# Optimization experiments

Measured on AMD Instinct MI355X. Metric: run time of the kernel, lower is better.

## Reference

```python
import jax, jax.numpy as jnp
import numpy as np

N = 50000
E = 400000
D = 128   # embed_dim == per-head out_channels
H = 2     # graph_heads
NEG_SLOPE = 0.2


def setup_inputs() -> dict:
    key = jax.random.key(0)
    ks = jax.random.split(key, 10)
    s = 1.0 / np.sqrt(D)
    x = jax.random.normal(ks[0], (N, D), dtype=jnp.float32)
    edge_index = jax.random.randint(ks[1], (2, E), 0, N, dtype=jnp.int64)
    # GATv2Conv params: lin_l (source), lin_r (target), attention vector, conv bias
    Wl = jax.random.uniform(ks[2], (H * D, D), jnp.float32, -s, s)
    bl = jax.random.uniform(ks[3], (H * D,), jnp.float32, -s, s)
    Wr = jax.random.uniform(ks[4], (H * D, D), jnp.float32, -s, s)
    br = jax.random.uniform(ks[5], (H * D,), jnp.float32, -s, s)
    att = jax.random.uniform(ks[6], (H, D), jnp.float32, -s, s)
    bias_conv = jnp.zeros((H * D,), jnp.float32)
    # trailing Linear(H*D -> D)
    so = 1.0 / np.sqrt(H * D)
    Wo = jax.random.uniform(ks[7], (D, H * D), jnp.float32, -so, so)
    bo = jax.random.uniform(ks[8], (D,), jnp.float32, -so, so)
    return {"x": x, "edge_index": edge_index, "Wl": Wl, "bl": bl, "Wr": Wr,
            "br": br, "att": att, "bias_conv": bias_conv, "Wo": Wo, "bo": bo}


def reference(x, edge_index, Wl, bl, Wr, br, att, bias_conv, Wo, bo):
    n = x.shape[0]
    # GATv2Conv default add_self_loops=True
    loops = jnp.arange(n, dtype=edge_index.dtype)
    src = jnp.concatenate([edge_index[0], loops])  # x_j (source / message)
    dst = jnp.concatenate([edge_index[1], loops])  # x_i (target / aggregation)

    xl = (x @ Wl.T + bl).reshape(n, H, D)  # source projection
    xr = (x @ Wr.T + br).reshape(n, H, D)  # target projection

    e = xl[src] + xr[dst]                               # [E+N, H, D]
    score = jnp.einsum('ehd,hd->eh', jax.nn.leaky_relu(e, NEG_SLOPE), att)

    # segment softmax over destination neighborhoods
    m = jax.ops.segment_max(score, dst, num_segments=n)  # [N, H]
    a = jnp.exp(score - m[dst])
    denom = jax.ops.segment_sum(a, dst, num_segments=n)
    alpha = a / (denom[dst] + 1e-16)                     # [E+N, H]

    out = jax.ops.segment_sum(xl[src] * alpha[..., None], dst, num_segments=n)
    out = out.reshape(n, H * D) + bias_conv              # concat heads + conv bias
    return out @ Wo.T + bo                               # [N, D]
```

## Files before the change

kernel.cpp:

```cpp
#include <hip/hip_runtime.h>
#include <math.h>

#define DIMV 128
#define HDV  256
#define NEGS 0.2f
#define CAPV 64

typedef __attribute__((ext_vector_type(8))) short short8;
typedef __attribute__((ext_vector_type(8))) unsigned short ushort8v;
typedef __attribute__((ext_vector_type(4))) float f32x4;

__device__ __forceinline__ int edge_at(const int* p, int is64, long long idx) {
    return is64 ? p[2 * idx] : p[(size_t)idx];
}

__device__ __forceinline__ unsigned short f2bf(float f) {
    union { float f; unsigned u; } v; v.f = f;
    unsigned r = (v.u + 0x7FFF + ((v.u >> 16) & 1)) >> 16;
    return (unsigned short)r;
}
__device__ __forceinline__ float bf2f(unsigned short b) {
    union { unsigned u; float f; } v; v.u = ((unsigned)b) << 16;
    return v.f;
}

__global__ __launch_bounds__(256) void build_prep_kernel(
    const int* __restrict__ eidx, int E, int nn,
    int* __restrict__ deg, int* __restrict__ elist,
    const float* __restrict__ Wl, const float* __restrict__ Wr,
    const float* __restrict__ Wo,
    unsigned short* __restrict__ WB, unsigned short* __restrict__ WoB)
{
    const int b = blockIdx.x, t = threadIdx.x;
    if (b < 128) {
        int tid = b * 256 + t;
        int f = tid * 2;
        int e    = f & 7;
        int rowc = (f >> 3) & 127;
        int lg   = (f >> 10) & 3;
        int kk   = (f >> 12) & 3;
        int mh   = f >> 14;
        int mat = mh >> 1, half = mh & 1;
        const float* W = mat ? Wr : Wl;
        float2 v = *(const float2*)(W + (size_t)(half * 128 + rowc) * DIMV + kk * 32 + lg * 8 + e);
        ushort2 o; o.x = f2bf(v.x); o.y = f2bf(v.y);
        *(ushort2*)(WB + f) = o;
    } else if (b < 192) {
        int tid = (b - 128) * 256 + t;
        int f = tid * 2;
        int e    = f & 7;
        int rowc = (f >> 3) & 127;
        int lg   = (f >> 10) & 3;
        int kk   = f >> 12;
        float2 v = *(const float2*)(Wo + (size_t)rowc * HDV + kk * 32 + lg * 8 + e);
        ushort2 o; o.x = f2bf(v.x); o.y = f2bf(v.y);
        *(ushort2*)(WoB + f) = o;
    } else {
        const int idx = (b - 192) * 256 + t;
        const int Et = E + nn;
        if (idx >= Et) return;
        const int is64 = ((eidx[1] | eidx[3] | eidx[5] | eidx[7]) == 0) ? 1 : 0;
        int s, d;
        if (idx < E) {
            s = edge_at(eidx, is64, idx);
            d = edge_at(eidx, is64, (long long)E + idx);
        } else {
            s = idx - E; d = s;
        }
        int pos = atomicAdd(deg + d, 1);
        if (pos < CAPV) elist[(size_t)d * CAPV + pos] = s;
    }
}

__global__ __launch_bounds__(512) void proj_mfma_kernel(
    const float* __restrict__ x,
    const unsigned short* __restrict__ WB,
    const float* __restrict__ bl, const float* __restrict__ br,
    unsigned short* __restrict__ xl, unsigned short* __restrict__ xr, int nn)
{
    __shared__ __align__(16) unsigned short buf[32768];
    const int t = threadIdx.x;
    const int m0b = blockIdx.x * 64;
    const int lane = t & 63, w8 = t >> 6;
    const int w = w8 & 3, half = w8 >> 2;
    const int lm = lane & 15, lg = lane >> 4;

    const int rowi = min(m0b + w * 16 + lm, nn - 1);
    const float* arow_p = x + (size_t)rowi * DIMV;
    short8 af[4];
#pragma unroll
    for (int kk = 0; kk < 4; ++kk) {
        float4 v0 = *(const float4*)(arow_p + kk * 32 + lg * 8);
        float4 v1 = *(const float4*)(arow_p + kk * 32 + lg * 8 + 4);
        short8 a;
        a[0] = (short)f2bf(v0.x); a[1] = (short)f2bf(v0.y);
        a[2] = (short)f2bf(v0.z); a[3] = (short)f2bf(v0.w);
        a[4] = (short)f2bf(v1.x); a[5] = (short)f2bf(v1.y);
        a[6] = (short)f2bf(v1.z); a[7] = (short)f2bf(v1.w);
        af[kk] = a;
    }

    f32x4 acc0[8], acc1[8];
#pragma unroll
    for (int nt = 0; nt < 8; ++nt) {
        acc0[nt] = (f32x4){0.f, 0.f, 0.f, 0.f};
        acc1[nt] = (f32x4){0.f, 0.f, 0.f, 0.f};
    }

    const unsigned short* myhalf = buf + half * 16384;

    {
        const ushort8v* src = (const ushort8v*)WB;
        ushort8v* dst = (ushort8v*)buf;
        for (int i = t; i < 4096; i += 512) dst[i] = src[i];
    }
    __syncthreads();
#pragma unroll
    for (int kk = 0; kk < 4; ++kk) {
        const unsigned short* wbL = myhalf + (kk * 4 + lg) * 1024;
#pragma unroll
        for (int nt = 0; nt < 8; ++nt) {
            short8 b0 = *(const short8*)(wbL + (nt * 16 + lm) * 8);
            acc0[nt] = __builtin_amdgcn_mfma_f32_16x16x32_bf16(af[kk], b0, acc0[nt], 0, 0, 0);
        }
    }
    __syncthreads();
    {
        const ushort8v* src = (const ushort8v*)(WB + 32768);
        ushort8v* dst = (ushort8v*)buf;
        for (int i = t; i < 4096; i += 512) dst[i] = src[i];
    }
    __syncthreads();
#pragma unroll
    for (int kk = 0; kk < 4; ++kk) {
        const unsigned short* wbL = myhalf + (kk * 4 + lg) * 1024;
#pragma unroll
        for (int nt = 0; nt < 8; ++nt) {
            short8 b1 = *(const short8*)(wbL + (nt * 16 + lm) * 8);
            acc1[nt] = __builtin_amdgcn_mfma_f32_16x16x32_bf16(af[kk], b1, acc1[nt], 0, 0, 0);
        }
    }
    __syncthreads();

    const int colbase = half * 128;
#pragma unroll
    for (int nt = 0; nt < 8; ++nt) {
        const int c = colbase + nt * 16 + lm;
        const float bv = bl[c];
#pragma unroll
        for (int rg = 0; rg < 4; ++rg)
            buf[(w * 16 + lg * 4 + rg) * 256 + c] = f2bf(acc0[nt][rg] + bv);
    }
    __syncthreads();
    for (int i = t; i < 64 * 32; i += 512) {
        int rr = i >> 5, q = i & 31;
        if (m0b + rr < nn)
            *(ushort8v*)(xl + (size_t)(m0b + rr) * HDV + q * 8) =
                *(const ushort8v*)(buf + rr * 256 + q * 8);
    }
    __syncthreads();
#pragma unroll
    for (int nt = 0; nt < 8; ++nt) {
        const int c = colbase + nt * 16 + lm;
        const float bv = br[c];
#pragma unroll
        for (int rg = 0; rg < 4; ++rg)
            buf[(w * 16 + lg * 4 + rg) * 256 + c] = f2bf(acc1[nt][rg] + bv);
    }
    __syncthreads();
    for (int i = t; i < 64 * 32; i += 512) {
        int rr = i >> 5, q = i & 31;
        if (m0b + rr < nn)
            *(ushort8v*)(xr + (size_t)(m0b + rr) * HDV + q * 8) =
                *(const ushort8v*)(buf + rr * 256 + q * 8);
    }
}

__global__ __launch_bounds__(256) void fused_kernel(
    const unsigned short* __restrict__ xl, const unsigned short* __restrict__ xr,
    const float* __restrict__ att,
    const int* __restrict__ deg, const int* __restrict__ elist,
    const float* __restrict__ bias_conv,
    const unsigned short* __restrict__ WoB, const float* __restrict__ bo,
    float* __restrict__ out, int nn)
{
    __shared__ __align__(16) unsigned short ags[16 * 256];
    const int t = threadIdx.x, lane = t & 63, wid = t >> 6;
    const int h = lane & 31, par = lane >> 5;
    const int n0 = blockIdx.x * 16;
    char* agsb = (char*)ags;
    float att8[8], bc8[8];
#pragma unroll
    for (int k = 0; k < 8; ++k) {
        att8[k] = att[h * 8 + k];
        bc8[k]  = bias_conv[h * 8 + k];
    }

    for (int j = 0; j < 4; ++j) {
        const int n = n0 + wid * 4 + j;
        const int r = wid * 4 + j;
        int dg = 0;
        const int* __restrict__ row = elist;
        float xr8[8];
#pragma unroll
        for (int k = 0; k < 8; ++k) xr8[k] = 0.f;
        if (n < nn) {
            dg = min(deg[n], CAPV);
            row = elist + (size_t)n * CAPV;
            ushort8v v = *(const ushort8v*)(xr + (size_t)n * HDV + h * 8);
#pragma unroll
            for (int k = 0; k < 8; ++k) xr8[k] = bf2f(v[k]);
        }
        const int myidx = row[lane];
        const int np = (dg + 1) >> 1, np1 = np - 1, dgm1 = dg - 1;
        float m0 = -1e30f, den = 0.f;
        float a8[8];
#pragma unroll
        for (int k = 0; k < 8; ++k) a8[k] = 0.f;

        if (np > 0) {
            int i0 = __shfl(myidx, min(par, dgm1), 64);
            int i1 = __shfl(myidx, min(2 * min(1, np1) + par, dgm1), 64);
            int i2 = __shfl(myidx, min(2 * min(2, np1) + par, dgm1), 64);
            int i3 = __shfl(myidx, min(2 * min(3, np1) + par, dgm1), 64);
            ushort8v v0 = *(const ushort8v*)(xl + (size_t)i0 * HDV + h * 8);
            ushort8v v1 = *(const ushort8v*)(xl + (size_t)i1 * HDV + h * 8);
            ushort8v v2 = *(const ushort8v*)(xl + (size_t)i2 * HDV + h * 8);
            ushort8v v3 = *(const ushort8v*)(xl + (size_t)i3 * HDV + h * 8);
            for (int ip = 0; ip < np; ++ip) {
                ushort8v cur = v0; v0 = v1; v1 = v2; v2 = v3;
                {
                    int pn = min(2 * min(ip + 4, np1) + par, dgm1);
                    int in_ = __shfl(myidx, pn, 64);
                    v3 = *(const ushort8v*)(xl + (size_t)in_ * HDV + h * 8);
                }
                float xv8[8];
#pragma unroll
                for (int k = 0; k < 8; ++k) xv8[k] = bf2f(cur[k]);
                float p = 0.f;
#pragma unroll
                for (int k = 0; k < 8; ++k) {
                    float e = xv8[k] + xr8[k];
                    e = fmaxf(e, NEGS * e);
                    p = fmaf(e, att8[k], p);
                }
                p += __shfl_xor(p, 1);
                p += __shfl_xor(p, 2);
                p += __shfl_xor(p, 4);
                p += __shfl_xor(p, 8);
                const bool valid = (2 * ip + par) < dg;
                if (!valid) p = -1e30f;
                if (p > m0) {
                    float sc = __expf(m0 - p);
                    den *= sc;
#pragma unroll
                    for (int k = 0; k < 8; ++k) a8[k] *= sc;
                    m0 = p;
                }
                float wgt = valid ? __expf(p - m0) : 0.f;
                den += wgt;
#pragma unroll
                for (int k = 0; k < 8; ++k) a8[k] = fmaf(wgt, xv8[k], a8[k]);
            }
        }
        float m1 = __shfl_xor(m0, 32);
        float d1 = __shfl_xor(den, 32);
        float mm = fmaxf(m0, m1);
        float s0 = __expf(m0 - mm);
        den = den * s0 + d1 * __expf(m1 - mm);
        float rden = 1.f / (den + 1e-16f);
        ushort8v o;
#pragma unroll
        for (int k = 0; k < 8; ++k) {
            float as = a8[k] * s0;
            as += __shfl_xor(as, 32);
            o[k] = f2bf(fmaf(as, rden, bc8[k]));
        }
        if (par == 0)
            *(ushort8v*)(agsb + ((r * 512 + h * 16) ^ ((r & 7) << 4))) = o;
    }
    __syncthreads();

    const int lm = lane & 15, lg = lane >> 4;
    f32x4 acc2[2];
    acc2[0] = (f32x4){0.f, 0.f, 0.f, 0.f};
    acc2[1] = (f32x4){0.f, 0.f, 0.f, 0.f};
    const int aswz = (lm & 7) << 4;
#pragma unroll
    for (int kk = 0; kk < 8; ++kk) {
        short8 afrag = *(const short8*)(agsb + ((lm * 512 + kk * 64 + lg * 16) ^ aswz));
        const unsigned short* wb = WoB + (size_t)((kk * 4 + lg) * 128) * 8;
#pragma unroll
        for (int u = 0; u < 2; ++u) {
            const int brow = (wid * 2 + u) * 16 + lm;
            short8 bfrag = *(const short8*)(wb + brow * 8);
            acc2[u] = __builtin_amdgcn_mfma_f32_16x16x32_bf16(afrag, bfrag, acc2[u], 0, 0, 0);
        }
    }
#pragma unroll
    for (int u = 0; u < 2; ++u) {
        const int c = (wid * 2 + u) * 16 + lm;
        const float bv = bo[c];
#pragma unroll
        for (int rg = 0; rg < 4; ++rg) {
            const int node = n0 + lg * 4 + rg;
            if (node < nn) out[(size_t)node * DIMV + c] = acc2[u][rg] + bv;
        }
    }
}

extern "C" void kernel_launch(void* const* d_in, const int* in_sizes, int n_in,
                              void* d_out, int out_size, void* d_ws, size_t ws_size,
                              hipStream_t stream) {
    const float* x         = (const float*)d_in[0];
    const int*   eidx      = (const int*)d_in[1];
    const float* Wl        = (const float*)d_in[2];
    const float* bl        = (const float*)d_in[3];
    const float* Wr        = (const float*)d_in[4];
    const float* br        = (const float*)d_in[5];
    const float* att       = (const float*)d_in[6];
    const float* bias_conv = (const float*)d_in[7];
    const float* Wo        = (const float*)d_in[8];
    const float* bo        = (const float*)d_in[9];
    float* out = (float*)d_out;

    const int nn = in_sizes[0] / DIMV;
    const int E  = in_sizes[1] / 2;
    const int Et = E + nn;

    char* ws = (char*)d_ws;
    size_t off = 0;
    auto alloc = [&](size_t bytes) -> void* {
        void* p = ws + off;
        off += (bytes + 255) & ~(size_t)255;
        return p;
    };
    unsigned short* xl  = (unsigned short*)alloc((size_t)nn * HDV * 2);
    unsigned short* xr  = (unsigned short*)alloc((size_t)nn * HDV * 2);
    int*   deg   = (int*)alloc((size_t)nn * 4);
    int*   elist = (int*)alloc((size_t)nn * CAPV * 4);
    unsigned short* WB  = (unsigned short*)alloc((size_t)65536 * 2);
    unsigned short* WoB = (unsigned short*)alloc((size_t)32768 * 2);
    (void)ws_size; (void)n_in; (void)out_size;

    hipMemsetAsync(deg, 0, (size_t)nn * 4, stream);

    const int EB = (Et + 255) / 256;
    build_prep_kernel<<<192 + EB, 256, 0, stream>>>(
        eidx, E, nn, deg, elist, Wl, Wr, Wo, WB, WoB);

    proj_mfma_kernel<<<(nn + 63) / 64, 512, 0, stream>>>(x, WB, bl, br, xl, xr, nn);

    fused_kernel<<<(nn + 15) / 16, 256, 0, stream>>>(xl, xr, att, deg, elist,
                                                     bias_conv, WoB, bo, out, nn);
}
```

Measured before the change: 129.5 us.

## Merge prep and projection kernels; drop max-subtraction in segment softmax

Combines the weight-conversion/edge-bucketing kernel with the projection GEMM kernel into one launch. Each projection block now converts Wl/Wr fp32 to bf16 straight into shared memory instead of reading a pre-converted buffer. Separately, the aggregation loop stops tracking a running max and rescaling, and exponentiates raw scores directly. This removes the per-edge branch and rescale work, but risks overflow or underflow in exp for large scores, a numerical assumption that depends on the input scale.

```diff
diff --git a/kernel.cpp b/kernel.cpp
--- a/kernel.cpp
+++ b/kernel.cpp
@@ -24,63 +24,49 @@
     return v.f;
 }
 
-__global__ __launch_bounds__(256) void build_prep_kernel(
-    const int* __restrict__ eidx, int E, int nn,
-    int* __restrict__ deg, int* __restrict__ elist,
+__global__ __launch_bounds__(512) void proj_prep_kernel(
+    const float* __restrict__ x,
     const float* __restrict__ Wl, const float* __restrict__ Wr,
     const float* __restrict__ Wo,
-    unsigned short* __restrict__ WB, unsigned short* __restrict__ WoB)
-{
-    const int b = blockIdx.x, t = threadIdx.x;
-    if (b < 128) {
-        int tid = b * 256 + t;
-        int f = tid * 2;
-        int e    = f & 7;
-        int rowc = (f >> 3) & 127;
-        int lg   = (f >> 10) & 3;
-        int kk   = (f >> 12) & 3;
-        int mh   = f >> 14;
-        int mat = mh >> 1, half = mh & 1;
-        const float* W = mat ? Wr : Wl;
-        float2 v = *(const float2*)(W + (size_t)(half * 128 + rowc) * DIMV + kk * 32 + lg * 8 + e);
-        ushort2 o; o.x = f2bf(v.x); o.y = f2bf(v.y);
-        *(ushort2*)(WB + f) = o;
-    } else if (b < 192) {
-        int tid = (b - 128) * 256 + t;
-        int f = tid * 2;
-        int e    = f & 7;
-        int rowc = (f >> 3) & 127;
-        int lg   = (f >> 10) & 3;
-        int kk   = f >> 12;
-        float2 v = *(const float2*)(Wo + (size_t)rowc * HDV + kk * 32 + lg * 8 + e);
-        ushort2 o; o.x = f2bf(v.x); o.y = f2bf(v.y);
-        *(ushort2*)(WoB + f) = o;
-    } else {
-        const int idx = (b - 192) * 256 + t;
-        const int Et = E + nn;
-        if (idx >= Et) return;
-        const int is64 = ((eidx[1] | eidx[3] | eidx[5] | eidx[7]) == 0) ? 1 : 0;
-        int s, d;
-        if (idx < E) {
-            s = edge_at(eidx, is64, idx);
-            d = edge_at(eidx, is64, (long long)E + idx);
-        } else {
-            s = idx - E; d = s;
-        }
-        int pos = atomicAdd(deg + d, 1);
-        if (pos < CAPV) elist[(size_t)d * CAPV + pos] = s;
-    }
-}
-
-__global__ __launch_bounds__(512) void proj_mfma_kernel(
-    const float* __restrict__ x,
-    const unsigned short* __restrict__ WB,
     const float* __restrict__ bl, const float* __restrict__ br,
-    unsigned short* __restrict__ xl, unsigned short* __restrict__ xr, int nn)
+    const int* __restrict__ eidx, int E, int nn, int PB,
+    int* __restrict__ deg, int* __restrict__ elist,
+    unsigned short* __restrict__ WoB,
+    unsigned short* __restrict__ xl, unsigned short* __restrict__ xr)
 {
     __shared__ __align__(16) unsigned short buf[32768];
-    const int t = threadIdx.x;
-    const int m0b = blockIdx.x * 64;
+    const int b = blockIdx.x, t = threadIdx.x;
+
+    if (b >= PB) {
+        if (b < PB + 32) {
+            int tid = (b - PB) * 512 + t;
+            int f = tid * 2;
+            int e    = f & 7;
+            int rowc = (f >> 3) & 127;
+            int lg   = (f >> 10) & 3;
+            int kk   = f >> 12;
+            float2 v = *(const float2*)(Wo + (size_t)rowc * HDV + kk * 32 + lg * 8 + e);
+            ushort2 o; o.x = f2bf(v.x); o.y = f2bf(v.y);
+            *(ushort2*)(WoB + f) = o;
+        } else {
+            const int idx = (b - PB - 32) * 512 + t;
+            const int Et = E + nn;
+            if (idx >= Et) return;
+            const int is64 = ((eidx[1] | eidx[3] | eidx[5] | eidx[7]) == 0) ? 1 : 0;
+            int s, d;
+            if (idx < E) {
+                s = edge_at(eidx, is64, idx);
+                d = edge_at(eidx, is64, (long long)E + idx);
+            } else {
+                s = idx - E; d = s;
+            }
+            int pos = atomicAdd(deg + d, 1);
+            if (pos < CAPV) elist[(size_t)d * CAPV + pos] = s;
+        }
+        return;
+    }
+
+    const int m0b = b * 64;
     const int lane = t & 63, w8 = t >> 6;
     const int w = w8 & 3, half = w8 >> 2;
     const int lm = lane & 15, lg = lane >> 4;
@@ -109,10 +95,18 @@
 
     const unsigned short* myhalf = buf + half * 16384;
 
-    {
-        const ushort8v* src = (const ushort8v*)WB;
-        ushort8v* dst = (ushort8v*)buf;
-        for (int i = t; i < 4096; i += 512) dst[i] = src[i];
+    for (int i = t; i < 4096; i += 512) {
+        int fs = i * 8;
+        int rowc = (fs >> 3) & 127;
+        int lgs  = (fs >> 10) & 3;
+        int kks  = (fs >> 12) & 3;
+        int hs   = (fs >> 14) & 1;
+        const float* src = Wl + (size_t)(hs * 128 + rowc) * DIMV + kks * 32 + lgs * 8;
+        float4 v0 = *(const float4*)src, v1 = *(const float4*)(src + 4);
+        ushort8v o;
+        o[0] = f2bf(v0.x); o[1] = f2bf(v0.y); o[2] = f2bf(v0.z); o[3] = f2bf(v0.w);
+        o[4] = f2bf(v1.x); o[5] = f2bf(v1.y); o[6] = f2bf(v1.z); o[7] = f2bf(v1.w);
+        *(ushort8v*)(buf + fs) = o;
     }
     __syncthreads();
 #pragma unroll
@@ -125,10 +119,18 @@
         }
     }
     __syncthreads();
-    {
-        const ushort8v* src = (const ushort8v*)(WB + 32768);
-        ushort8v* dst = (ushort8v*)buf;
-        for (int i = t; i < 4096; i += 512) dst[i] = src[i];
+    for (int i = t; i < 4096; i += 512) {
+        int fs = i * 8;
+        int rowc = (fs >> 3) & 127;
+        int lgs  = (fs >> 10) & 3;
+        int kks  = (fs >> 12) & 3;
+        int hs   = (fs >> 14) & 1;
+        const float* src = Wr + (size_t)(hs * 128 + rowc) * DIMV + kks * 32 + lgs * 8;
+        float4 v0 = *(const float4*)src, v1 = *(const float4*)(src + 4);
+        ushort8v o;
+        o[0] = f2bf(v0.x); o[1] = f2bf(v0.y); o[2] = f2bf(v0.z); o[3] = f2bf(v0.w);
+        o[4] = f2bf(v1.x); o[5] = f2bf(v1.y); o[6] = f2bf(v1.z); o[7] = f2bf(v1.w);
+        *(ushort8v*)(buf + fs) = o;
     }
     __syncthreads();
 #pragma unroll
@@ -213,7 +215,7 @@
         }
         const int myidx = row[lane];
         const int np = (dg + 1) >> 1, np1 = np - 1, dgm1 = dg - 1;
-        float m0 = -1e30f, den = 0.f;
+        float den = 0.f;
         float a8[8];
 #pragma unroll
         for (int k = 0; k < 8; ++k) a8[k] = 0.f;
@@ -249,31 +251,18 @@
                 p += __shfl_xor(p, 4);
                 p += __shfl_xor(p, 8);
                 const bool valid = (2 * ip + par) < dg;
-                if (!valid) p = -1e30f;
-                if (p > m0) {
-                    float sc = __expf(m0 - p);
-                    den *= sc;
-#pragma unroll
-                    for (int k = 0; k < 8; ++k) a8[k] *= sc;
-                    m0 = p;
-                }
-                float wgt = valid ? __expf(p - m0) : 0.f;
+                float wgt = valid ? __expf(p) : 0.f;
                 den += wgt;
 #pragma unroll
                 for (int k = 0; k < 8; ++k) a8[k] = fmaf(wgt, xv8[k], a8[k]);
             }
         }
-        float m1 = __shfl_xor(m0, 32);
-        float d1 = __shfl_xor(den, 32);
-        float mm = fmaxf(m0, m1);
-        float s0 = __expf(m0 - mm);
-        den = den * s0 + d1 * __expf(m1 - mm);
+        den += __shfl_xor(den, 32);
         float rden = 1.f / (den + 1e-16f);
         ushort8v o;
 #pragma unroll
         for (int k = 0; k < 8; ++k) {
-            float as = a8[k] * s0;
-            as += __shfl_xor(as, 32);
+            float as = a8[k] + __shfl_xor(a8[k], 32);
             o[k] = f2bf(fmaf(as, rden, bc8[k]));
         }
         if (par == 0)
@@ -339,17 +328,15 @@
     unsigned short* xr  = (unsigned short*)alloc((size_t)nn * HDV * 2);
     int*   deg   = (int*)alloc((size_t)nn * 4);
     int*   elist = (int*)alloc((size_t)nn * CAPV * 4);
-    unsigned short* WB  = (unsigned short*)alloc((size_t)65536 * 2);
     unsigned short* WoB = (unsigned short*)alloc((size_t)32768 * 2);
     (void)ws_size; (void)n_in; (void)out_size;
 
     hipMemsetAsync(deg, 0, (size_t)nn * 4, stream);
 
-    const int EB = (Et + 255) / 256;
-    build_prep_kernel<<<192 + EB, 256, 0, stream>>>(
-        eidx, E, nn, deg, elist, Wl, Wr, Wo, WB, WoB);
-
-    proj_mfma_kernel<<<(nn + 63) / 64, 512, 0, stream>>>(x, WB, bl, br, xl, xr, nn);
+    const int PB  = (nn + 63) / 64;
+    const int EBK = (Et + 511) / 512;
+    proj_prep_kernel<<<PB + 32 + EBK, 512, 0, stream>>>(
+        x, Wl, Wr, Wo, bl, br, eidx, E, nn, PB, deg, elist, WoB, xl, xr);
 
     fused_kernel<<<(nn + 15) / 16, 256, 0, stream>>>(xl, xr, att, deg, elist,
                                                      bias_conv, WoB, bo, out, nn);
```

Measured after the change: 152.3 us. 1.18x slower.
